# Kernel optimization log

Measured on AMD Instinct MI355X. Metric: run time of the kernel, lower is better.

The kernel has to match this reference:

```python
import jax, jax.numpy as jnp
import numpy as np

# KWConv2d config: in=256, out=256, k=3, s=1, p=1, groups=1, bias=False
# warehouse: 32 spatial cells of shape [64, 64, 3, 3]; num_fourier_basis=0; temp_value=0
B, CIN, H, W_ = 32, 256, 56, 56
OUT = 256
NUM_CELLS, CO, CI, KH, KW = 32, 64, 64, 3, 3
HIDDEN = 16                 # max(int(256 * 0.0625), 16)
GO, GI, GS = OUT // CO, CIN // CI, 1
M = GO * GI * GS            # num_local_mixture = 16
P = NUM_CELLS + 1           # kw_planes_per_mixture = 33
KWP = P * M                 # kw_planes = 528


def setup_inputs() -> dict:
    key = jax.random.key(0)
    ks = jax.random.split(key, 4)
    s = 0.02
    return {
        "x": jax.random.normal(ks[0], (B, CIN, H, W_), jnp.float32),
        "cells": jax.random.normal(ks[1], (NUM_CELLS, CO, CI, KH, KW), jnp.float32) * s,
        "fc1_w": jax.random.normal(ks[2], (HIDDEN, CIN), jnp.float32) * s,
        "fc1_b": jnp.zeros((HIDDEN,), jnp.float32),
        "ln_g": jnp.ones((HIDDEN,), jnp.float32),
        "ln_b": jnp.zeros((HIDDEN,), jnp.float32),
        "sp_w": jax.random.normal(ks[3], (KWP, HIDDEN), jnp.float32) * s,
        "sp_b": jnp.zeros((KWP,), jnp.float32),
    }


def _attention(x, fc1_w, fc1_b, ln_g, ln_b, sp_w, sp_b):
    # AdaptiveAvgPool1d(1) over flattened spatial dims == global mean
    pooled = x.mean(axis=(2, 3))                      # [B, CIN]
    h = pooled @ fc1_w.T + fc1_b                      # [B, HIDDEN]
    mu = h.mean(-1, keepdims=True)
    var = ((h - mu) ** 2).mean(-1, keepdims=True)
    h = (h - mu) * jax.lax.rsqrt(var + 1e-5) * ln_g + ln_b
    h = jax.nn.relu(h)
    a = h @ sp_w.T + sp_b                             # spatial_head -> [B, KWP]
    a = a.reshape(-1, P)                              # [B*M, P]
    a = a / (jnp.abs(a).sum(axis=1, keepdims=True) + 0.001)  # L1 normalize per mixture
    # temp_value = 0 -> attention unchanged; drop last (zero) column
    return a[:, :-1]                                  # [B*M, NUM_CELLS]


def reference(x, cells, fc1_w, fc1_b, ln_g, ln_b, sp_w, sp_b):
    att = _attention(x, fc1_w, fc1_b, ln_g, ln_b, sp_w, sp_b)  # [B*M, NUM_CELLS]
    w = cells.reshape(NUM_CELLS, -1)                  # [NUM_CELLS, CO*CI*KH*KW]
    agg = att @ w                                     # [B*M, CO*CI*KH*KW]
    agg = agg.reshape(B, GS, GO, GI, CO, CI, KH, KW)
    agg = agg.transpose(0, 2, 4, 3, 5, 1, 6, 7)       # torch permute (0,2,4,3,5,1,6,7)
    agg = agg.reshape(B * OUT, CIN, KH, KW)           # per-sample kernels (groups=1)
    # grouped-conv trick: fold batch into channels, groups = B
    xr = x.reshape(1, B * CIN, H, W_)
    out = jax.lax.conv_general_dilated(
        xr, agg, window_strides=(1, 1), padding=((1, 1), (1, 1)),
        dimension_numbers=("NCHW", "OIHW", "NCHW"), feature_group_count=B)
    return out.reshape(B, OUT, H, W_)
```

## Files before the change

kernel.cpp:

```cpp
#include <hip/hip_runtime.h>
#include <stdint.h>

typedef unsigned short ush;
typedef __bf16   bf16x8 __attribute__((ext_vector_type(8)));
typedef float    f32x4  __attribute__((ext_vector_type(4)));
typedef uint32_t u32x4  __attribute__((ext_vector_type(4)));

union U16B { u32x4 u; bf16x8 b; };
union P8   { ush us[8]; u32x4 v; };

template<int V> struct ICx { static constexpr int value = V; };

__device__ __forceinline__ ush f2bf(float f) {
    union { float f; uint32_t u; } v; v.f = f;
    uint32_t r = v.u + 0x7FFFu + ((v.u >> 16) & 1u);
    return (ush)(r >> 16);
}

__device__ __forceinline__ void gl_lds16(const ush* g, ush* l) {
    __builtin_amdgcn_global_load_lds(
        (const __attribute__((address_space(1))) uint32_t*)g,
        (__attribute__((address_space(3))) uint32_t*)l, 16, 0, 0);
}

#define HWPX  3136
#define POOL_OFF   58720256UL
#define ATT_OFF    58753024UL
#define WAGG_OFF   58818560UL

__global__ void k_transpose(const float* __restrict__ x, ush* __restrict__ xT,
                            float* __restrict__ pooled) {
    __shared__ float tile[64][65];
    int blk = blockIdx.x;
    int b   = blk / 196;
    int rem = blk % 196;
    int icg = rem / 49;
    int pxg = rem % 49;
    int t = threadIdx.x;

    {
        int icl  = t >> 2, part = t & 3;
        const float* src = x + (size_t)(b * 256 + icg * 64 + icl) * HWPX + pxg * 64 + part * 16;
        #pragma unroll
        for (int k = 0; k < 4; ++k) {
            f32x4 v = *(const f32x4*)(src + k * 4);
            tile[icl][part * 16 + k * 4 + 0] = v[0];
            tile[icl][part * 16 + k * 4 + 1] = v[1];
            tile[icl][part * 16 + k * 4 + 2] = v[2];
            tile[icl][part * 16 + k * 4 + 3] = v[3];
        }
    }

    if (t < 32) {
        int r = (pxg * 64 + 55) / 56 + (t >> 4);
        if (r < 56 && r * 56 <= pxg * 64 + 63) {
            int icg32 = icg * 2 + ((t >> 3) & 1);
            int colp  = ((t >> 2) & 1) ? 57 : 0;
            int chunk = t & 3;
            u32x4 z = (u32x4)(0u);
            *(u32x4*)(xT + (((size_t)(b * 8 + icg32) * 56 + r) * 64 + colp) * 32 + chunk * 8) = z;
        }
    }
    __syncthreads();

    if (t < 64) {
        float s = 0.f;
        #pragma unroll 8
        for (int p = 0; p < 64; ++p) s += tile[t][p];
        atomicAdd(pooled + b * 256 + icg * 64 + t, s);
    }

    {
        int pxl = t >> 2, icq = t & 3;
        int px  = pxg * 64 + pxl;
        int row = px / 56;
        int col = px - row * 56;
        int p   = col + 1;
        int xorp = (p >> 1) & 3;
        int icg32   = icg * 2 + (icq >> 1);
        int subbase = (icq & 1) * 2;
        P8 lo, hi;
        #pragma unroll
        for (int m = 0; m < 8; ++m) {
            lo.us[m] = f2bf(tile[icq * 16 + m][pxl]);
            hi.us[m] = f2bf(tile[icq * 16 + 8 + m][pxl]);
        }
        size_t base = (((size_t)(b * 8 + icg32) * 56 + row) * 64 + p) * 32;
        *(u32x4*)(xT + base + (size_t)((subbase ^ xorp) * 8))       = lo.v;
        *(u32x4*)(xT + base + (size_t)(((subbase + 1) ^ xorp) * 8)) = hi.v;
    }
}

__global__ void k_attn(const float* __restrict__ pooled,
                       const float* __restrict__ fc1_w, const float* __restrict__ fc1_b,
                       const float* __restrict__ ln_g,  const float* __restrict__ ln_b,
                       const float* __restrict__ sp_w,  const float* __restrict__ sp_b,
                       float* __restrict__ att) {
    __shared__ float hs[32][16];
    int t = threadIdx.x;
    {
        int b = t >> 4, j = t & 15;
        float acc = 0.f;
        for (int c = 0; c < 256; ++c) acc += pooled[b * 256 + c] * fc1_w[j * 256 + c];
        hs[b][j] = fc1_b[j] + acc * (1.0f / 3136.0f);
    }
    __syncthreads();
    if (t < 32) {
        float mu = 0.f;
        #pragma unroll
        for (int j = 0; j < 16; ++j) mu += hs[t][j];
        mu *= (1.0f / 16.0f);
        float var = 0.f;
        #pragma unroll
        for (int j = 0; j < 16; ++j) { float d = hs[t][j] - mu; var += d * d; }
        var *= (1.0f / 16.0f);
        float inv = rsqrtf(var + 1e-5f);
        #pragma unroll
        for (int j = 0; j < 16; ++j) {
            float v = (hs[t][j] - mu) * inv * ln_g[j] + ln_b[j];
            hs[t][j] = fmaxf(v, 0.f);
        }
    }
    __syncthreads();
    {
        int b = t >> 4, m = t & 15;
        float a[33];
        #pragma unroll 1
        for (int i = 0; i < 33; ++i) {
            int p = m * 33 + i;
            float acc = sp_b[p];
            #pragma unroll
            for (int j = 0; j < 16; ++j) acc += hs[b][j] * sp_w[p * 16 + j];
            a[i] = acc;
        }
        float s = 0.f;
        #pragma unroll
        for (int i = 0; i < 33; ++i) s += fabsf(a[i]);
        float inv = 1.0f / (s + 0.001f);
        #pragma unroll
        for (int c = 0; c < 32; ++c) att[(b * 16 + m) * 32 + c] = a[c] * inv;
    }
}

__global__ void k_agg(const float* __restrict__ cells, const float* __restrict__ att,
                      ush* __restrict__ wagg) {
    __shared__ float at[512];
    int blk = blockIdx.x;
    int b = blk >> 6, co = blk & 63;
    int t = threadIdx.x;
    for (int i = t; i < 512; i += 256) at[i] = att[b * 512 + i];
    __syncthreads();
    int ci = t & 63, gi = t >> 6;
    float acc[4][9];
    #pragma unroll
    for (int g = 0; g < 4; ++g)
        #pragma unroll
        for (int k = 0; k < 9; ++k) acc[g][k] = 0.f;
    for (int c = 0; c < 32; ++c) {
        float a0 = at[(0 + gi) * 32 + c];
        float a1 = at[(4 + gi) * 32 + c];
        float a2 = at[(8 + gi) * 32 + c];
        float a3 = at[(12 + gi) * 32 + c];
        const float* cp = cells + (size_t)c * 36864 + co * 576 + ci * 9;
        #pragma unroll
        for (int k = 0; k < 9; ++k) {
            float cv = cp[k];
            acc[0][k] += a0 * cv; acc[1][k] += a1 * cv;
            acc[2][k] += a2 * cv; acc[3][k] += a3 * cv;
        }
    }
    int ic  = gi * 64 + ci;
    int cc  = ic >> 5;
    int s   = (ic >> 3) & 3;
    int icw = ic & 7;
    #pragma unroll
    for (int g = 0; g < 4; ++g)
        #pragma unroll
        for (int k = 0; k < 9; ++k)
            wagg[((size_t)(b * 32 + cc * 4 + g) * 9 + k) * 2048 + s * 512 + co * 8 + icw]
                = f2bf(acc[g][k]);
}

__global__ __launch_bounds__(256, 2) void k_conv(const ush* __restrict__ xT,
                                                 const ush* __restrict__ wagg,
                                                 float* __restrict__ out) {
    __shared__ __align__(16) ush xs[2][12288];
    __shared__ __align__(16) ush wsh[2][8192];

    int tid = threadIdx.x;
    int wg  = blockIdx.x;
    int xcd = wg & 7;
    int kk  = wg >> 3;
    int gq  = kk / 14;
    int sp  = kk - gq * 14;
    int g   = gq * 8 + xcd;
    int b   = g >> 2, octile = g & 3;
    int row0 = sp * 4, oc0 = octile * 64;

    int lane = tid & 63, w = tid >> 6;
    int wn = w & 1, ocH = w >> 1;
    int l15 = lane & 15, s4 = lane >> 4;

    {
        u32x4 z = (u32x4)(0u);
        #pragma unroll
        for (int i = 0; i < 12; ++i) ((u32x4*)xs)[tid + i * 256] = z;
    }

    int prow[7], pq[7];
    #pragma unroll
    for (int j = 0; j < 7; ++j) {
        int px = wn * 112 + j * 16 + l15;
        prow[j] = px / 56;
        pq[j]   = px - prow[j] * 56;
    }

    unsigned vmask = 0;
    #pragma unroll
    for (int k = 0; k < 6; ++k) {
        int grow = row0 - 1 + k;
        if (grow >= 0 && grow < 56) vmask |= 1u << k;
    }
    const bool full6 = (vmask == 0x3Fu);

    const ush* wc0 = wagg + ((size_t)b * 32 + octile) * 9 * 2048;
    const int  woff = s4 * 512 + (ocH * 32 + l15) * 8;
    const ush* w8gl = wc0 + 8 * 2048 + woff;
    const ush* xb = xT + (size_t)b * 8 * 56 * 2048 + (size_t)tid * 8;

    f32x4 acc[2][7];
    #pragma unroll
    for (int mi = 0; mi < 2; ++mi)
        #pragma unroll
        for (int j = 0; j < 7; ++j) acc[mi][j] = (f32x4)(0.f);

    __syncthreads();

    #pragma unroll
    for (int k = 0; k < 4; ++k)
        gl_lds16(wc0 + (w * 4 + k) * 512 + lane * 8, &wsh[0][(w * 4 + k) * 512]);
    #pragma unroll
    for (int k = 0; k < 6; ++k)
        if (vmask & (1u << k))
            gl_lds16(xb + (size_t)(row0 - 1 + k) * 2048, &xs[0][k * 2048 + w * 512]);
    __syncthreads();

    auto do_tap = [&](const ush* xsb, const ush* wfp, int dy, int dx) {
        U16B wf[2];
        wf[0].u = *(const u32x4*)(wfp);
        wf[1].u = *(const u32x4*)(wfp + 128);
        U16B bx[7];
        #pragma unroll
        for (int j = 0; j < 7; ++j) {
            int q    = pq[j] + dx;
            int slot = s4 ^ ((q >> 1) & 3);
            bx[j].u = *(const u32x4*)(xsb + ((prow[j] + dy) * 64 + q) * 32 + slot * 8);
        }
        __builtin_amdgcn_s_setprio(1);
        #pragma unroll
        for (int j = 0; j < 7; ++j) {
            acc[0][j] = __builtin_amdgcn_mfma_f32_16x16x32_bf16(bx[j].b, wf[0].b, acc[0][j], 0, 0, 0);
            acc[1][j] = __builtin_amdgcn_mfma_f32_16x16x32_bf16(bx[j].b, wf[1].b, acc[1][j], 0, 0, 0);
        }
        __builtin_amdgcn_s_setprio(0);
    };

    auto chunk_body = [&](auto parc, int cc) {
        constexpr int PAR = decltype(parc)::value;
        const ush* xsb = &xs[PAR][0];
        const ush* wck = wc0 + (size_t)cc * 73728;

        U16B wf8[2];
        wf8[0].u = *(const u32x4*)(w8gl + (size_t)cc * 73728);
        wf8[1].u = *(const u32x4*)(w8gl + (size_t)cc * 73728 + 128);
        #pragma unroll
        for (int k = 0; k < 4; ++k)
            gl_lds16(wck + 8192 + (w * 4 + k) * 512 + lane * 8,
                     &wsh[1][(w * 4 + k) * 512]);
        __builtin_amdgcn_sched_barrier(0);
        if (cc < 7) {
            #pragma unroll
            for (int k = 0; k < 6; ++k)
                if (vmask & (1u << k))
                    gl_lds16(xb + (size_t)((cc + 1) * 56 + row0 - 1 + k) * 2048,
                             &xs[PAR ^ 1][k * 2048 + w * 512]);
        }
        do_tap(xsb, &wsh[0][0 * 2048 + woff], 0, 0);
        do_tap(xsb, &wsh[0][1 * 2048 + woff], 0, 1);
        do_tap(xsb, &wsh[0][2 * 2048 + woff], 0, 2);
        do_tap(xsb, &wsh[0][3 * 2048 + woff], 1, 0);
        asm volatile("s_waitcnt lgkmcnt(0)" ::: "memory");
        if (cc < 7) {
            if (full6) asm volatile("s_waitcnt vmcnt(6)" ::: "memory");
            else       asm volatile("s_waitcnt vmcnt(5)" ::: "memory");
        } else {
            asm volatile("s_waitcnt vmcnt(0)" ::: "memory");
        }
        __builtin_amdgcn_s_barrier();

        if (cc < 7) {
            #pragma unroll
            for (int k = 0; k < 4; ++k)
                gl_lds16(wck + 73728 + (w * 4 + k) * 512 + lane * 8,
                         &wsh[0][(w * 4 + k) * 512]);
        }
        do_tap(xsb, &wsh[1][0 * 2048 + woff], 1, 1);
        do_tap(xsb, &wsh[1][1 * 2048 + woff], 1, 2);
        do_tap(xsb, &wsh[1][2 * 2048 + woff], 2, 0);
        do_tap(xsb, &wsh[1][3 * 2048 + woff], 2, 1);
        {
            U16B bx[7];
            #pragma unroll
            for (int j = 0; j < 7; ++j) {
                int q    = pq[j] + 2;
                int slot = s4 ^ ((q >> 1) & 3);
                bx[j].u = *(const u32x4*)(xsb + ((prow[j] + 2) * 64 + q) * 32 + slot * 8);
            }
            __builtin_amdgcn_s_setprio(1);
            #pragma unroll
            for (int j = 0; j < 7; ++j) {
                acc[0][j] = __builtin_amdgcn_mfma_f32_16x16x32_bf16(bx[j].b, wf8[0].b, acc[0][j], 0, 0, 0);
                acc[1][j] = __builtin_amdgcn_mfma_f32_16x16x32_bf16(bx[j].b, wf8[1].b, acc[1][j], 0, 0, 0);
            }
            __builtin_amdgcn_s_setprio(0);
        }
        asm volatile("s_waitcnt lgkmcnt(0)" ::: "memory");
        asm volatile("s_waitcnt vmcnt(0)" ::: "memory");
        __builtin_amdgcn_s_barrier();
    };

    for (int c2 = 0; c2 < 8; c2 += 2) {
        chunk_body(ICx<0>{}, c2);
        chunk_body(ICx<1>{}, c2 + 1);
    }

    int pxbase = row0 * 56 + wn * 112 + s4 * 4;
    #pragma unroll
    for (int mi = 0; mi < 2; ++mi) {
        int oc = oc0 + ocH * 32 + mi * 16 + l15;
        float* o = out + (size_t)(b * 256 + oc) * HWPX + pxbase;
        #pragma unroll
        for (int j = 0; j < 7; ++j)
            *(f32x4*)(o + j * 16) = acc[mi][j];
    }
}

extern "C" void kernel_launch(void* const* d_in, const int* in_sizes, int n_in,
                              void* d_out, int out_size, void* d_ws, size_t ws_size,
                              hipStream_t stream) {
    const float* x     = (const float*)d_in[0];
    const float* cells = (const float*)d_in[1];
    const float* fc1_w = (const float*)d_in[2];
    const float* fc1_b = (const float*)d_in[3];
    const float* ln_g  = (const float*)d_in[4];
    const float* ln_b  = (const float*)d_in[5];
    const float* sp_w  = (const float*)d_in[6];
    const float* sp_b  = (const float*)d_in[7];
    float* out = (float*)d_out;

    char* ws = (char*)d_ws;
    ush*   xT     = (ush*)ws;
    float* pooled = (float*)(ws + POOL_OFF);
    float* att    = (float*)(ws + ATT_OFF);
    ush*   wagg   = (ush*)(ws + WAGG_OFF);

    hipMemsetAsync(pooled, 0, 32768, stream);
    k_transpose<<<6272, 256, 0, stream>>>(x, xT, pooled);
    k_attn<<<1, 512, 0, stream>>>(pooled, fc1_w, fc1_b, ln_g, ln_b, sp_w, sp_b, att);
    k_agg<<<2048, 256, 0, stream>>>(cells, att, wagg);
    k_conv<<<1792, 256, 0, stream>>>(xT, wagg, out);
}
```

Baseline: 237.4 us.

## Widen conv output-channel tile to 128 to halve input-tile reloads

Result: no change. 237.5 us (+0.1%).

```diff
diff --git a/kernel.cpp b/kernel.cpp
--- a/kernel.cpp
+++ b/kernel.cpp
@@ -194,8 +194,8 @@
     int gq  = kk / 14;
     int sp  = kk - gq * 14;
     int g   = gq * 8 + xcd;
-    int b   = g >> 2, octile = g & 3;
-    int row0 = sp * 4, oc0 = octile * 64;
+    int b   = g >> 1, octile = g & 1;
+    int row0 = sp * 4, oc0 = octile * 128;
 
     int lane = tid & 63, w = tid >> 6;
     int wn = w & 1, ocH = w >> 1;
@@ -223,32 +223,33 @@
     }
     const bool full6 = (vmask == 0x3Fu);
 
-    const ush* wc0 = wagg + ((size_t)b * 32 + octile) * 9 * 2048;
-    const int  woff = s4 * 512 + (ocH * 32 + l15) * 8;
-    const ush* w8gl = wc0 + 8 * 2048 + woff;
+    const ush* wc0 = wagg + ((size_t)b * 32 + octile * 2) * 18432;
+    const int  woff = s4 * 1024 + ocH * 512 + l15 * 8;
+    const ush* w8gl = wc0 + (size_t)ocH * 18432 + 8 * 2048 + s4 * 512 + l15 * 8;
     const ush* xb = xT + (size_t)b * 8 * 56 * 2048 + (size_t)tid * 8;
 
-    f32x4 acc[2][7];
-    #pragma unroll
-    for (int mi = 0; mi < 2; ++mi)
+    f32x4 acc[4][7];
+    #pragma unroll
+    for (int mi = 0; mi < 4; ++mi)
         #pragma unroll
         for (int j = 0; j < 7; ++j) acc[mi][j] = (f32x4)(0.f);
 
-    __syncthreads();
-
-    #pragma unroll
-    for (int k = 0; k < 4; ++k)
-        gl_lds16(wc0 + (w * 4 + k) * 512 + lane * 8, &wsh[0][(w * 4 + k) * 512]);
-    #pragma unroll
-    for (int k = 0; k < 6; ++k)
-        if (vmask & (1u << k))
-            gl_lds16(xb + (size_t)(row0 - 1 + k) * 2048, &xs[0][k * 2048 + w * 512]);
-    __syncthreads();
+    auto wdma = [&](int cc2, int tapbase, int half) {
+        const ush* base = wc0 + (size_t)cc2 * 73728;
+        ush* dst = &wsh[half][0];
+        #pragma unroll
+        for (int k = 0; k < 4; ++k) {
+            int p  = w * 4 + k;
+            int tl = p >> 3, sl = (p >> 1) & 3, oh = p & 1;
+            gl_lds16(base + (size_t)oh * 18432 + (size_t)(tapbase + tl) * 2048 + sl * 512 + lane * 8,
+                     dst + tl * 4096 + sl * 1024 + oh * 512);
+        }
+    };
 
     auto do_tap = [&](const ush* xsb, const ush* wfp, int dy, int dx) {
-        U16B wf[2];
-        wf[0].u = *(const u32x4*)(wfp);
-        wf[1].u = *(const u32x4*)(wfp + 128);
+        U16B wf[4];
+        #pragma unroll
+        for (int mi = 0; mi < 4; ++mi) wf[mi].u = *(const u32x4*)(wfp + mi * 128);
         U16B bx[7];
         #pragma unroll
         for (int j = 0; j < 7; ++j) {
@@ -261,22 +262,46 @@
         for (int j = 0; j < 7; ++j) {
             acc[0][j] = __builtin_amdgcn_mfma_f32_16x16x32_bf16(bx[j].b, wf[0].b, acc[0][j], 0, 0, 0);
             acc[1][j] = __builtin_amdgcn_mfma_f32_16x16x32_bf16(bx[j].b, wf[1].b, acc[1][j], 0, 0, 0);
+            acc[2][j] = __builtin_amdgcn_mfma_f32_16x16x32_bf16(bx[j].b, wf[2].b, acc[2][j], 0, 0, 0);
+            acc[3][j] = __builtin_amdgcn_mfma_f32_16x16x32_bf16(bx[j].b, wf[3].b, acc[3][j], 0, 0, 0);
         }
         __builtin_amdgcn_s_setprio(0);
     };
+
+    __syncthreads();
+
+    wdma(0, 0, 0);
+    #pragma unroll
+    for (int k = 0; k < 6; ++k)
+        if (vmask & (1u << k))
+            gl_lds16(xb + (size_t)(row0 - 1 + k) * 2048, &xs[0][k * 2048 + w * 512]);
+    __syncthreads();
 
     auto chunk_body = [&](auto parc, int cc) {
         constexpr int PAR = decltype(parc)::value;
         const ush* xsb = &xs[PAR][0];
-        const ush* wck = wc0 + (size_t)cc * 73728;
-
-        U16B wf8[2];
-        wf8[0].u = *(const u32x4*)(w8gl + (size_t)cc * 73728);
-        wf8[1].u = *(const u32x4*)(w8gl + (size_t)cc * 73728 + 128);
-        #pragma unroll
-        for (int k = 0; k < 4; ++k)
-            gl_lds16(wck + 8192 + (w * 4 + k) * 512 + lane * 8,
-                     &wsh[1][(w * 4 + k) * 512]);
+
+        wdma(cc, 2, 1);
+        do_tap(xsb, &wsh[0][0 * 4096 + woff], 0, 0);
+        do_tap(xsb, &wsh[0][1 * 4096 + woff], 0, 1);
+        asm volatile("s_waitcnt lgkmcnt(0)" ::: "memory");
+        asm volatile("s_waitcnt vmcnt(0)" ::: "memory");
+        __builtin_amdgcn_s_barrier();
+
+        wdma(cc, 4, 0);
+        do_tap(xsb, &wsh[1][0 * 4096 + woff], 0, 2);
+        do_tap(xsb, &wsh[1][1 * 4096 + woff], 1, 0);
+        asm volatile("s_waitcnt lgkmcnt(0)" ::: "memory");
+        asm volatile("s_waitcnt vmcnt(0)" ::: "memory");
+        __builtin_amdgcn_s_barrier();
+
+        U16B wf8[4];
+        {
+            const ush* w8 = w8gl + (size_t)cc * 73728;
+            #pragma unroll
+            for (int mi = 0; mi < 4; ++mi) wf8[mi].u = *(const u32x4*)(w8 + mi * 128);
+        }
+        wdma(cc, 6, 1);
         __builtin_amdgcn_sched_barrier(0);
         if (cc < 7) {
             #pragma unroll
@@ -285,10 +310,9 @@
                     gl_lds16(xb + (size_t)((cc + 1) * 56 + row0 - 1 + k) * 2048,
                              &xs[PAR ^ 1][k * 2048 + w * 512]);
         }
-        do_tap(xsb, &wsh[0][0 * 2048 + woff], 0, 0);
-        do_tap(xsb, &wsh[0][1 * 2048 + woff], 0, 1);
-        do_tap(xsb, &wsh[0][2 * 2048 + woff], 0, 2);
-        do_tap(xsb, &wsh[0][3 * 2048 + woff], 1, 0);
+        __builtin_amdgcn_sched_barrier(0);
+        do_tap(xsb, &wsh[0][0 * 4096 + woff], 1, 1);
+        do_tap(xsb, &wsh[0][1 * 4096 + woff], 1, 2);
         asm volatile("s_waitcnt lgkmcnt(0)" ::: "memory");
         if (cc < 7) {
             if (full6) asm volatile("s_waitcnt vmcnt(6)" ::: "memory");
@@ -298,16 +322,9 @@
         }
         __builtin_amdgcn_s_barrier();
 
-        if (cc < 7) {
-            #pragma unroll
-            for (int k = 0; k < 4; ++k)
-                gl_lds16(wck + 73728 + (w * 4 + k) * 512 + lane * 8,
-                         &wsh[0][(w * 4 + k) * 512]);
-        }
-        do_tap(xsb, &wsh[1][0 * 2048 + woff], 1, 1);
-        do_tap(xsb, &wsh[1][1 * 2048 + woff], 1, 2);
-        do_tap(xsb, &wsh[1][2 * 2048 + woff], 2, 0);
-        do_tap(xsb, &wsh[1][3 * 2048 + woff], 2, 1);
+        if (cc < 7) wdma(cc + 1, 0, 0);
+        do_tap(xsb, &wsh[1][0 * 4096 + woff], 2, 0);
+        do_tap(xsb, &wsh[1][1 * 4096 + woff], 2, 1);
         {
             U16B bx[7];
             #pragma unroll
@@ -321,6 +338,8 @@
             for (int j = 0; j < 7; ++j) {
                 acc[0][j] = __builtin_amdgcn_mfma_f32_16x16x32_bf16(bx[j].b, wf8[0].b, acc[0][j], 0, 0, 0);
                 acc[1][j] = __builtin_amdgcn_mfma_f32_16x16x32_bf16(bx[j].b, wf8[1].b, acc[1][j], 0, 0, 0);
+                acc[2][j] = __builtin_amdgcn_mfma_f32_16x16x32_bf16(bx[j].b, wf8[2].b, acc[2][j], 0, 0, 0);
+                acc[3][j] = __builtin_amdgcn_mfma_f32_16x16x32_bf16(bx[j].b, wf8[3].b, acc[3][j], 0, 0, 0);
             }
             __builtin_amdgcn_s_setprio(0);
         }
@@ -336,8 +355,8 @@
 
     int pxbase = row0 * 56 + wn * 112 + s4 * 4;
     #pragma unroll
-    for (int mi = 0; mi < 2; ++mi) {
-        int oc = oc0 + ocH * 32 + mi * 16 + l15;
+    for (int mi = 0; mi < 4; ++mi) {
+        int oc = oc0 + ocH * 64 + mi * 16 + l15;
         float* o = out + (size_t)(b * 256 + oc) * HWPX + pxbase;
         #pragma unroll
         for (int j = 0; j < 7; ++j)
@@ -368,5 +387,5 @@
     k_transpose<<<6272, 256, 0, stream>>>(x, xT, pooled);
     k_attn<<<1, 512, 0, stream>>>(pooled, fc1_w, fc1_b, ln_g, ln_b, sp_w, sp_b, att);
     k_agg<<<2048, 256, 0, stream>>>(cells, att, wagg);
-    k_conv<<<1792, 256, 0, stream>>>(xT, wagg, out);
-}
+    k_conv<<<896, 256, 0, stream>>>(xT, wagg, out);
+}
```
